# Kernel optimization log

Hardware: AMD Instinct MI355X
Metric: run time of the kernel (lower is better)

Reference implementation:

```python
import jax, jax.numpy as jnp
import numpy as np

V, DM, DEPTH, N = 50257, 512, 8, 16  # vocab, dim, depth, ssm_dim
B, L = 2, 1024
GATE = 0.5  # fixed_gate=True blend


def layer_norm(x, g, b):
    mu = x.mean(-1, keepdims=True)
    xm = x - mu
    var = (xm * xm).mean(-1, keepdims=True)
    return xm * jax.lax.rsqrt(var + 1e-5) * g + b


def ssm(u, W_dt, b_dt, W_B, W_C, A_log, D_p):
    # selective SSM: h_t = exp(dt_t*A)*h_{t-1} + dt_t*B_t*u_t ; y_t = C_t.h_t + D*u_t
    dt = jax.nn.softplus(u @ W_dt + b_dt)            # (B,L,DM)
    Bm = u @ W_B                                      # (B,L,N)
    Cm = u @ W_C                                      # (B,L,N)
    A = -jnp.exp(A_log)                               # (DM,N), stable (negative)

    def step(h, inp):
        dt_t, B_t, C_t, u_t = inp                     # (B,DM),(B,N),(B,N),(B,DM)
        h = jnp.exp(dt_t[..., None] * A) * h + (dt_t * u_t)[..., None] * B_t[:, None, :]
        y = jnp.einsum('bdn,bn->bd', h, C_t)
        return h, y

    h0 = jnp.zeros((u.shape[0], DM, N), u.dtype)
    xs = (dt.transpose(1, 0, 2), Bm.transpose(1, 0, 2), Cm.transpose(1, 0, 2), u.transpose(1, 0, 2))
    _, ys = jax.lax.scan(step, h0, xs)
    return ys.transpose(1, 0, 2) + D_p * u


def wkv(x, W_r, W_k, W_v, W_o, t_decay, t_first):
    # RWKV-4 channel-wise WKV recurrence
    r = jax.nn.sigmoid(x @ W_r)
    k = jnp.clip(x @ W_k, -30.0, 30.0)
    v = x @ W_v
    w = jnp.exp(-jnp.exp(t_decay))                    # (DM,) decay in (0,1)

    def step(carry, inp):
        a, b = carry
        k_t, v_t = inp
        ek = jnp.exp(k_t)
        eu = jnp.exp(t_first + k_t)
        out = (a + eu * v_t) / (b + eu + 1e-6)
        return (w * a + ek * v_t, w * b + ek), out

    a0 = jnp.zeros((x.shape[0], DM), x.dtype)
    _, o = jax.lax.scan(step, (a0, jnp.zeros_like(a0)), (k.transpose(1, 0, 2), v.transpose(1, 0, 2)))
    return (r * o.transpose(1, 0, 2)) @ W_o


def setup_inputs() -> dict:
    key = jax.random.key(0)
    ks = jax.random.split(key, 16)
    s = 0.02
    inp = {
        'input_ids': jax.random.randint(ks[0], (B, L), 0, V, dtype=jnp.int32),
        'emb': jax.random.normal(ks[1], (V, DM), jnp.float32) * s,
        'ln1_g': jnp.ones((DEPTH, DM), jnp.float32),
        'ln1_b': jnp.zeros((DEPTH, DM), jnp.float32),
        'W_dt': jax.random.normal(ks[2], (DEPTH, DM, DM), jnp.float32) * s,
        'b_dt': jnp.zeros((DEPTH, DM), jnp.float32),
        'W_B': jax.random.normal(ks[3], (DEPTH, DM, N), jnp.float32) * s,
        'W_C': jax.random.normal(ks[4], (DEPTH, DM, N), jnp.float32) * s,
        'A_log': jnp.broadcast_to(jnp.log(jnp.arange(1, N + 1, dtype=jnp.float32)), (DEPTH, DM, N)).copy(),
        'D_p': jnp.ones((DEPTH, DM), jnp.float32),
        'ln2_g': jnp.ones((DEPTH, DM), jnp.float32),
        'ln2_b': jnp.zeros((DEPTH, DM), jnp.float32),
        'W_r': jax.random.normal(ks[5], (DEPTH, DM, DM), jnp.float32) * s,
        'W_k': jax.random.normal(ks[6], (DEPTH, DM, DM), jnp.float32) * s,
        'W_v': jax.random.normal(ks[7], (DEPTH, DM, DM), jnp.float32) * s,
        'W_o': jax.random.normal(ks[8], (DEPTH, DM, DM), jnp.float32) * s,
        't_decay': jax.random.normal(ks[9], (DEPTH, DM), jnp.float32) * 0.5,
        't_first': jax.random.normal(ks[10], (DEPTH, DM), jnp.float32) * 0.5,
        'lnf_g': jnp.ones((DM,), jnp.float32),
        'lnf_b': jnp.zeros((DM,), jnp.float32),
    }
    return inp


def reference(input_ids, emb, ln1_g, ln1_b, W_dt, b_dt, W_B, W_C, A_log, D_p,
              ln2_g, ln2_b, W_r, W_k, W_v, W_o, t_decay, t_first, lnf_g, lnf_b):
    x = emb[input_ids]                                # (B,L,DM)
    for i in range(DEPTH):
        x = x + GATE * ssm(layer_norm(x, ln1_g[i], ln1_b[i]),
                           W_dt[i], b_dt[i], W_B[i], W_C[i], A_log[i], D_p[i])
        x = x + GATE * wkv(layer_norm(x, ln2_g[i], ln2_b[i]),
                           W_r[i], W_k[i], W_v[i], W_o[i], t_decay[i], t_first[i])
    x = layer_norm(x, lnf_g, lnf_b)
    logits = x @ emb.T                                # tied LM head, (B,L,V)
    return logits
```

## Files before the change

kernel.cpp:

```cpp
#include <hip/hip_runtime.h>

#define DM 512
#define NST 16
#define NDEPTH 8
#define NB 2
#define NL 1024
#define MROWS 2048
#define VOCAB 50257
#define VPAD  50304
#define NCH 32
#define CLEN 32

typedef __attribute__((ext_vector_type(8))) short bf16x8;
typedef __attribute__((ext_vector_type(4))) float f32x4;
typedef __attribute__((ext_vector_type(8))) unsigned short ushort8;

#define AS1(p) ((const __attribute__((address_space(1))) void*)(p))
#define AS3(p) ((__attribute__((address_space(3))) void*)(p))

static __device__ __forceinline__ unsigned short f2bf(float f) {
  unsigned int x = __float_as_uint(f);
  unsigned int r = (x + 0x7FFFu + ((x >> 16) & 1u)) >> 16;
  return (unsigned short)r;
}
static __device__ __forceinline__ float bf2f(unsigned short u) {
  return __uint_as_float((unsigned int)u << 16);
}

__global__ __launch_bounds__(256) void k_gather(const int* __restrict__ ids,
    const float* __restrict__ emb, float* __restrict__ x)
{
  int gid = blockIdx.x * 256 + threadIdx.x;
  int row = gid >> 7, c = (gid & 127) * 4;
  int id = ids[row];
  *(float4*)(x + (size_t)row * DM + c) = *(const float4*)(emb + (size_t)id * DM + c);
}

__global__ void k_transpose(const float* __restrict__ Wdt, const float* __restrict__ Wr,
    const float* __restrict__ Wk, const float* __restrict__ Wv, const float* __restrict__ Wo,
    unsigned short* __restrict__ Tdtbc, unsigned short* __restrict__ Trkv, unsigned short* __restrict__ To)
{
  __shared__ float tile[32][33];
  int z = blockIdx.z, layer = z / 5, f = z % 5;
  const float* src;
  unsigned short* dst;
  size_t lw = (size_t)layer * DM * DM;
  if (f == 0)      { src = Wdt + lw; dst = Tdtbc + (size_t)layer * 640 * DM; }
  else if (f == 1) { src = Wr  + lw; dst = Trkv + (size_t)layer * 3 * DM * DM; }
  else if (f == 2) { src = Wk  + lw; dst = Trkv + (size_t)layer * 3 * DM * DM + DM * DM; }
  else if (f == 3) { src = Wv  + lw; dst = Trkv + (size_t)layer * 3 * DM * DM + 2 * DM * DM; }
  else             { src = Wo  + lw; dst = To   + lw; }
  int tx = threadIdx.x, ty = threadIdx.y;
  int kb = blockIdx.y * 32, nb = blockIdx.x * 32;
  #pragma unroll
  for (int i = 0; i < 4; i++)
    tile[ty + i * 8][tx] = src[(size_t)(kb + ty + i * 8) * DM + nb + tx];
  __syncthreads();
  #pragma unroll
  for (int i = 0; i < 4; i++)
    dst[(size_t)(nb + ty + i * 8) * DM + kb + tx] = f2bf(tile[tx][ty + i * 8]);
}

__global__ __launch_bounds__(256) void k_bcpack(const float* __restrict__ WB,
    const float* __restrict__ WC, unsigned short* __restrict__ Tdtbc)
{
  int gid = blockIdx.x * 256 + threadIdx.x;
  int k = gid & 511, n = (gid >> 9) & 127, layer = gid >> 16;
  float v = 0.f;
  if (n < 16)      v = WB[((size_t)layer * DM + k) * NST + n];
  else if (n < 32) v = WC[((size_t)layer * DM + k) * NST + (n - 16)];
  Tdtbc[(size_t)layer * 640 * DM + (size_t)(512 + n) * DM + k] = f2bf(v);
}

__global__ __launch_bounds__(256) void k_embcvt(const float* __restrict__ emb,
    unsigned short* __restrict__ out)
{
  int gid = blockIdx.x * 256 + threadIdx.x;
  size_t base = (size_t)gid * 8;
  int row = (int)(base >> 9);
  ushort8 o;
  if (row < VOCAB) {
    float4 a = *(const float4*)(emb + base);
    float4 b = *(const float4*)(emb + base + 4);
    o[0]=f2bf(a.x); o[1]=f2bf(a.y); o[2]=f2bf(a.z); o[3]=f2bf(a.w);
    o[4]=f2bf(b.x); o[5]=f2bf(b.y); o[6]=f2bf(b.z); o[7]=f2bf(b.w);
  } else {
    o = (ushort8)0;
  }
  *(ushort8*)(out + base) = o;
}

__global__ __launch_bounds__(256) void k_ln(const float* __restrict__ x,
    const float* __restrict__ g, const float* __restrict__ bb,
    float* __restrict__ of, unsigned short* __restrict__ ob)
{
  const int w = threadIdx.x >> 6, l = threadIdx.x & 63;
  const int row = blockIdx.x * 4 + w;
  const float* xr = x + (size_t)row * DM + l * 8;
  float4 v0 = *(const float4*)(xr);
  float4 v1 = *(const float4*)(xr + 4);
  float s = v0.x + v0.y + v0.z + v0.w + v1.x + v1.y + v1.z + v1.w;
  float q = v0.x*v0.x + v0.y*v0.y + v0.z*v0.z + v0.w*v0.w
          + v1.x*v1.x + v1.y*v1.y + v1.z*v1.z + v1.w*v1.w;
  #pragma unroll
  for (int m = 1; m < 64; m <<= 1) { s += __shfl_xor(s, m); q += __shfl_xor(q, m); }
  const float mu = s * (1.0f / DM);
  const float var = q * (1.0f / DM) - mu * mu;
  const float rs = rsqrtf(var + 1e-5f);
  const float4 g0 = *(const float4*)(g + l * 8);
  const float4 g1 = *(const float4*)(g + l * 8 + 4);
  const float4 b0 = *(const float4*)(bb + l * 8);
  const float4 b1 = *(const float4*)(bb + l * 8 + 4);
  float y[8];
  y[0] = (v0.x - mu) * rs * g0.x + b0.x;
  y[1] = (v0.y - mu) * rs * g0.y + b0.y;
  y[2] = (v0.z - mu) * rs * g0.z + b0.z;
  y[3] = (v0.w - mu) * rs * g0.w + b0.w;
  y[4] = (v1.x - mu) * rs * g1.x + b1.x;
  y[5] = (v1.y - mu) * rs * g1.y + b1.y;
  y[6] = (v1.z - mu) * rs * g1.z + b1.z;
  y[7] = (v1.w - mu) * rs * g1.w + b1.w;
  if (of) {
    float4 o0 = {y[0], y[1], y[2], y[3]}, o1 = {y[4], y[5], y[6], y[7]};
    *(float4*)(of + (size_t)row * DM + l * 8) = o0;
    *(float4*)(of + (size_t)row * DM + l * 8 + 4) = o1;
  }
  if (ob) {
    ushort8 o;
    #pragma unroll
    for (int j = 0; j < 8; j++) o[j] = f2bf(y[j]);
    *(ushort8*)(ob + (size_t)row * DM + l * 8) = o;
  }
}

template<int BM, int BN, int EPI>
__global__ __launch_bounds__(256) void gemm_bt(const unsigned short* __restrict__ A,
    const unsigned short* __restrict__ Bt, float* __restrict__ C, int N, int ldc,
    const float* __restrict__ bias, float* __restrict__ C2)
{
  constexpr int K = DM;
  constexpr int MI = BM / 32, NI = BN / 32;
  __shared__ unsigned short lsA0[BM * 64];
  __shared__ unsigned short lsA1[BM * 64];
  __shared__ unsigned short lsB0[BN * 64];
  __shared__ unsigned short lsB1[BN * 64];
  const int t = threadIdx.x;
  const int w = t >> 6, l = t & 63;
  const int wm = (w >> 1) * (BM / 2), wn = (w & 1) * (BN / 2);
  const size_t bm = (size_t)blockIdx.x * BM, bn = (size_t)blockIdx.y * BN;
  f32x4 acc[MI][NI] = {};
  const int srow = t >> 3, sslot = t & 7;
  const int gs = sslot ^ (srow & 7);
  const unsigned short* Ag = A + (bm + srow) * K + gs * 8;
  const unsigned short* Bg = Bt + (bn + srow) * K + gs * 8;
  const int lr = l & 15, lq = l >> 4;

#define GB_STAGE(dA, dB, kt) do {                                              \
    const int k0_ = (kt) * 64;                                                 \
    _Pragma("unroll")                                                          \
    for (int o = 0; o < BM / 32; ++o)                                          \
      __builtin_amdgcn_global_load_lds(AS1(Ag + (size_t)(o * 32) * K + k0_),   \
          AS3(dA + (o * 32 + srow) * 64 + sslot * 8), 16, 0, 0);               \
    _Pragma("unroll")                                                          \
    for (int o = 0; o < BN / 32; ++o)                                          \
      __builtin_amdgcn_global_load_lds(AS1(Bg + (size_t)(o * 32) * K + k0_),   \
          AS3(dB + (o * 32 + srow) * 64 + sslot * 8), 16, 0, 0);               \
  } while (0)

#define GB_COMPUTE(sA, sB) do {                                                \
    bf16x8 af[MI][2], bfr[NI][2];                                              \
    _Pragma("unroll")                                                          \
    for (int i = 0; i < MI; ++i) {                                             \
      int row = wm + i * 16 + lr;                                              \
      _Pragma("unroll")                                                        \
      for (int h = 0; h < 2; ++h)                                              \
        af[i][h] = *(const bf16x8*)(sA + row * 64 + (((h * 4 + lq) ^ (row & 7)) * 8)); \
    }                                                                          \
    _Pragma("unroll")                                                          \
    for (int i = 0; i < NI; ++i) {                                             \
      int row = wn + i * 16 + lr;                                              \
      _Pragma("unroll")                                                        \
      for (int h = 0; h < 2; ++h)                                              \
        bfr[i][h] = *(const bf16x8*)(sB + row * 64 + (((h * 4 + lq) ^ (row & 7)) * 8)); \
    }                                                                          \
    _Pragma("unroll")                                                          \
    for (int h = 0; h < 2; ++h)                                                \
      _Pragma("unroll")                                                        \
      for (int mi = 0; mi < MI; ++mi)                                          \
        _Pragma("unroll")                                                      \
        for (int ni = 0; ni < NI; ++ni)                                        \
          acc[mi][ni] = __builtin_amdgcn_mfma_f32_16x16x32_bf16(af[mi][h], bfr[ni][h], acc[mi][ni], 0, 0, 0); \
  } while (0)

  GB_STAGE(lsA0, lsB0, 0);
  __syncthreads();
  #pragma unroll
  for (int kk = 0; kk < 4; ++kk) {
    GB_STAGE(lsA1, lsB1, kk * 2 + 1);
    GB_COMPUTE(lsA0, lsB0);
    __syncthreads();
    if (kk * 2 + 2 < 8) GB_STAGE(lsA0, lsB0, kk * 2 + 2);
    GB_COMPUTE(lsA1, lsB1);
    __syncthreads();
  }
#undef GB_STAGE
#undef GB_COMPUTE

  const int lg = l >> 4;
  #pragma unroll
  for (int mi = 0; mi < MI; ++mi) {
    #pragma unroll
    for (int ni = 0; ni < NI; ++ni) {
      int n = (int)bn + wn + ni * 16 + lr;
      size_t m0 = bm + wm + mi * 16 + lg * 4;
      #pragma unroll
      for (int j = 0; j < 4; ++j) {
        float v = acc[mi][ni][j];
        if (EPI == 0) {
          C[(m0 + j) * (size_t)ldc + n] = v;
        } else if (EPI == 2) {
          C2[(m0 + j) * (size_t)ldc + n] += 0.5f * v;
        } else {
          if (n < 512) {
            float b = v + bias[n];
            C[(m0 + j) * (size_t)512 + n] = fmaxf(b, 0.f) + log1pf(__expf(-fabsf(b)));
          } else if (n < 544) {
            C2[(m0 + j) * (size_t)32 + (n - 512)] = v;
          }
        }
      }
    }
  }
}

__global__ __launch_bounds__(512) void gemm_head(const unsigned short* __restrict__ A,
    const unsigned short* __restrict__ Bt, float* __restrict__ C)
{
  __shared__ unsigned short lsA[256 * 64];
  __shared__ unsigned short lsB[128 * 64];
  const int t = threadIdx.x;
  const int w = t >> 6, l = t & 63;
  const int wm = (w >> 1) * 64, wn = (w & 1) * 64;
  const int c = (int)blockIdx.x & 7, j = (int)blockIdx.x >> 3;
  const int ntile = c * 50 + (j >> 3), mtile = j & 7;
  if (ntile >= 393) return;
  const size_t bm = (size_t)mtile * 256, bn = (size_t)ntile * 128;
  f32x4 acc[4][4] = {};
  const int srow = t >> 3, sslot = t & 7;
  const int gs = sslot ^ (srow & 7);
  const unsigned short* Ag = A + (bm + srow) * DM + gs * 8;
  const unsigned short* Bg = Bt + (bn + srow) * DM + gs * 8;
  const int lr = l & 15, lq = l >> 4;
  for (int k0 = 0; k0 < DM; k0 += 64) {
    #pragma unroll
    for (int o = 0; o < 4; ++o)
      __builtin_amdgcn_global_load_lds(AS1(Ag + (size_t)(o * 64) * DM + k0),
          AS3(lsA + (o * 64 + srow) * 64 + sslot * 8), 16, 0, 0);
    #pragma unroll
    for (int o = 0; o < 2; ++o)
      __builtin_amdgcn_global_load_lds(AS1(Bg + (size_t)(o * 64) * DM + k0),
          AS3(lsB + (o * 64 + srow) * 64 + sslot * 8), 16, 0, 0);
    asm volatile("s_waitcnt vmcnt(0)" ::: "memory");
    __syncthreads();
    bf16x8 af[4][2], bfr[4][2];
    #pragma unroll
    for (int i = 0; i < 4; ++i) {
      int row = wm + i * 16 + lr;
      #pragma unroll
      for (int h = 0; h < 2; ++h)
        af[i][h] = *(const bf16x8*)(lsA + row * 64 + (((h * 4 + lq) ^ (row & 7)) * 8));
    }
    #pragma unroll
    for (int i = 0; i < 4; ++i) {
      int row = wn + i * 16 + lr;
      #pragma unroll
      for (int h = 0; h < 2; ++h)
        bfr[i][h] = *(const bf16x8*)(lsB + row * 64 + (((h * 4 + lq) ^ (row & 7)) * 8));
    }
    #pragma unroll
    for (int h = 0; h < 2; ++h)
      #pragma unroll
      for (int mi = 0; mi < 4; ++mi)
        #pragma unroll
        for (int ni = 0; ni < 4; ++ni)
          acc[mi][ni] = __builtin_amdgcn_mfma_f32_16x16x32_bf16(af[mi][h], bfr[ni][h], acc[mi][ni], 0, 0, 0);
    __syncthreads();
  }
  const int lg = l >> 4;
  #pragma unroll
  for (int mi = 0; mi < 4; ++mi) {
    #pragma unroll
    for (int ni = 0; ni < 4; ++ni) {
      int n = (int)bn + wn + ni * 16 + lr;
      if (n >= VOCAB) continue;
      size_t m0 = bm + wm + mi * 16 + lg * 4;
      #pragma unroll
      for (int jj = 0; jj < 4; ++jj)
        C[(m0 + jj) * (size_t)VOCAB + n] = acc[mi][ni][jj];
    }
  }
}

__global__ __launch_bounds__(256) void k_ssm1(const float* __restrict__ dt,
    const unsigned short* __restrict__ u, const float* __restrict__ BC,
    const float* __restrict__ A_log, float* __restrict__ Pb, float* __restrict__ Sb)
{
  const int t = threadIdx.x;
  const int grp = t >> 4, n = t & 15;
  const int cg = blockIdx.x & 63, ck = blockIdx.x >> 6;
  const int ch = cg * 16 + grp;
  const int b = ch >> 9, d = ch & 511;
  const float A = -__expf(A_log[d * NST + n]);
  const int t0 = ck * CLEN;
  const float* dtp = dt + ((size_t)b * NL + t0) * DM + d;
  const unsigned short* up = u + ((size_t)b * NL + t0) * DM + d;
  const float* bcp = BC + ((size_t)b * NL + t0) * 32 + n;
  float P = 1.f, S = 0.f;
  #pragma unroll
  for (int tt = 0; tt < CLEN; ++tt) {
    float dtv = dtp[(size_t)tt * DM];
    float uv  = bf2f(up[(size_t)tt * DM]);
    float Bv  = bcp[(size_t)tt * 32];
    float e = __expf(dtv * A);
    S = fmaf(e, S, dtv * uv * Bv);
    P *= e;
  }
  size_t cn = (size_t)ch * NST + n;
  Pb[cn * NCH + ck] = P;
  Sb[cn * NCH + ck] = S;
}

__global__ __launch_bounds__(256) void k_ssm2(const float* __restrict__ Pb,
    const float* __restrict__ Sb, float* __restrict__ H0)
{
  const int wid = blockIdx.x * 8 + (threadIdx.x >> 5);
  const int lane = threadIdx.x & 31;
  float coef = Pb[(size_t)wid * NCH + lane];
  float sum  = Sb[(size_t)wid * NCH + lane];
  #pragma unroll
  for (int m = 1; m < 32; m <<= 1) {
    float cr = __shfl_up(coef, m, 32);
    float sr = __shfl_up(sum, m, 32);
    if (lane >= m) { sum = fmaf(coef, sr, sum); coef *= cr; }
  }
  float hp = __shfl_up(sum, 1, 32);
  H0[(size_t)wid * NCH + lane] = (lane == 0) ? 0.f : hp;
}

__global__ __launch_bounds__(256) void k_ssm3(const float* __restrict__ dt,
    const unsigned short* __restrict__ u, const float* __restrict__ BC,
    const float* __restrict__ A_log, const float* __restrict__ Dp,
    const float* __restrict__ H0, float* __restrict__ x)
{
  const int t = threadIdx.x;
  const int grp = t >> 4, n = t & 15;
  const int cg = blockIdx.x & 63, ck = blockIdx.x >> 6;
  const int ch = cg * 16 + grp;
  const int b = ch >> 9, d = ch & 511;
  const float A = -__expf(A_log[d * NST + n]);
  const float Dpv = Dp[d];
  const int t0 = ck * CLEN;
  const float* dtp = dt + ((size_t)b * NL + t0) * DM + d;
  const unsigned short* up = u + ((size_t)b * NL + t0) * DM + d;
  const float* bcp = BC + ((size_t)b * NL + t0) * 32 + n;
  float* xp = x + ((size_t)b * NL + t0) * DM + d;
  size_t cn = (size_t)ch * NST + n;
  float h = H0[cn * NCH + ck];
  #pragma unroll
  for (int tt = 0; tt < CLEN; ++tt) {
    float dtv = dtp[(size_t)tt * DM];
    float uv  = bf2f(up[(size_t)tt * DM]);
    float Bv  = bcp[(size_t)tt * 32];
    float Cv  = bcp[(size_t)tt * 32 + 16];
    float e = __expf(dtv * A);
    h = fmaf(e, h, dtv * uv * Bv);
    float p2 = h * Cv;
    p2 += __shfl_xor(p2, 1);
    p2 += __shfl_xor(p2, 2);
    p2 += __shfl_xor(p2, 4);
    p2 += __shfl_xor(p2, 8);
    if (n == 0) xp[(size_t)tt * DM] += 0.5f * (p2 + Dpv * uv);
  }
}

__global__ __launch_bounds__(256) void k_wkv1(const float* __restrict__ rkv,
    const float* __restrict__ tdec, float* __restrict__ SaB, float* __restrict__ SbB)
{
  const int gid = blockIdx.x * 256 + threadIdx.x;
  const int ch = gid & 1023, ck = gid >> 10;
  const int b = ch >> 9, d = ch & 511;
  const float w = __expf(-__expf(tdec[d]));
  const float* base = rkv + ((size_t)b * NL + ck * CLEN) * 1536;
  float Sa = 0.f, Sb = 0.f;
  #pragma unroll
  for (int tt = 0; tt < CLEN; ++tt) {
    const float* row = base + (size_t)tt * 1536;
    float kt = row[512 + d];
    kt = fminf(30.f, fmaxf(-30.f, kt));
    float vt = row[1024 + d];
    float ek = __expf(kt);
    Sa = fmaf(w, Sa, ek * vt);
    Sb = fmaf(w, Sb, ek);
  }
  SaB[(size_t)ch * NCH + ck] = Sa;
  SbB[(size_t)ch * NCH + ck] = Sb;
}

__global__ __launch_bounds__(256) void k_wkv2(const float* __restrict__ SaB,
    const float* __restrict__ SbB, const float* __restrict__ tdec,
    float* __restrict__ HaB, float* __restrict__ HbB)
{
  const int ch = blockIdx.x * 8 + (threadIdx.x >> 5);
  const int lane = threadIdx.x & 31;
  const int d = ch & 511;
  float coef = __expf(-32.f * __expf(tdec[d]));
  float sa = SaB[(size_t)ch * NCH + lane];
  float sb = SbB[(size_t)ch * NCH + lane];
  #pragma unroll
  for (int m = 1; m < 32; m <<= 1) {
    float cr  = __shfl_up(coef, m, 32);
    float sar = __shfl_up(sa, m, 32);
    float sbr = __shfl_up(sb, m, 32);
    if (lane >= m) { sa = fmaf(coef, sar, sa); sb = fmaf(coef, sbr, sb); coef *= cr; }
  }
  float ha = __shfl_up(sa, 1, 32);
  float hb = __shfl_up(sb, 1, 32);
  HaB[(size_t)ch * NCH + lane] = (lane == 0) ? 0.f : ha;
  HbB[(size_t)ch * NCH + lane] = (lane == 0) ? 0.f : hb;
}

__global__ __launch_bounds__(256) void k_wkv3(const float* __restrict__ rkv,
    const float* __restrict__ tdec, const float* __restrict__ tfir,
    const float* __restrict__ HaB, const float* __restrict__ HbB,
    unsigned short* __restrict__ ro)
{
  const int gid = blockIdx.x * 256 + threadIdx.x;
  const int ch = gid & 1023, ck = gid >> 10;
  const int b = ch >> 9, d = ch & 511;
  const float w = __expf(-__expf(tdec[d]));
  const float tf = tfir[d];
  float a = HaB[(size_t)ch * NCH + ck];
  float bden = HbB[(size_t)ch * NCH + ck];
  const int t0 = ck * CLEN;
  const float* base = rkv + ((size_t)b * NL + t0) * 1536;
  unsigned short* rop = ro + ((size_t)b * NL + t0) * DM + d;
  #pragma unroll
  for (int tt = 0; tt < CLEN; ++tt) {
    const float* row = base + (size_t)tt * 1536;
    float rv = row[d];
    float kt = row[512 + d];
    kt = fminf(30.f, fmaxf(-30.f, kt));
    float vt = row[1024 + d];
    float ek = __expf(kt);
    float eu = __expf(tf + kt);
    float out = __fdividef(a + eu * vt, bden + eu + 1e-6f);
    float sig = __fdividef(1.f, 1.f + __expf(-rv));
    rop[(size_t)tt * DM] = f2bf(sig * out);
    a = fmaf(w, a, ek * vt);
    bden = fmaf(w, bden, ek);
  }
}

extern "C" void kernel_launch(void* const* d_in, const int* in_sizes, int n_in,
                              void* d_out, int out_size, void* d_ws, size_t ws_size,
                              hipStream_t stream)
{
  const int*   ids   = (const int*)d_in[0];
  const float* emb   = (const float*)d_in[1];
  const float* ln1_g = (const float*)d_in[2];
  const float* ln1_b = (const float*)d_in[3];
  const float* W_dt  = (const float*)d_in[4];
  const float* b_dt  = (const float*)d_in[5];
  const float* W_B   = (const float*)d_in[6];
  const float* W_C   = (const float*)d_in[7];
  const float* A_log = (const float*)d_in[8];
  const float* D_p   = (const float*)d_in[9];
  const float* ln2_g = (const float*)d_in[10];
  const float* ln2_b = (const float*)d_in[11];
  const float* W_r   = (const float*)d_in[12];
  const float* W_k   = (const float*)d_in[13];
  const float* W_v   = (const float*)d_in[14];
  const float* W_o   = (const float*)d_in[15];
  const float* t_dec = (const float*)d_in[16];
  const float* t_fir = (const float*)d_in[17];
  const float* lnf_g = (const float*)d_in[18];
  const float* lnf_b = (const float*)d_in[19];

  char* p = (char*)d_ws;
  float*          xres  = (float*)(p + 0);
  float*          dtb   = (float*)(p + 8388608);
  float*          rkv   = (float*)(p + 12582912);
  float*          BCb   = (float*)(p + 25165824);
  unsigned short* abuf  = (unsigned short*)(p + 25427968);
  unsigned short* Tdtbc = (unsigned short*)(p + 27525120);
  unsigned short* To    = (unsigned short*)(p + 32768000);
  unsigned short* Trkv  = (unsigned short*)(p + 36962304);
  unsigned short* Tem   = (unsigned short*)(p + 49545216);

  float* Pb  = rkv;
  float* Sb  = rkv + 524288;
  float* H0  = rkv + 1048576;
  float* SaB = dtb;
  float* SbB = dtb + 32768;
  float* HaB = dtb + 65536;
  float* HbB = dtb + 98304;

  k_gather<<<1024, 256, 0, stream>>>(ids, emb, xres);
  k_transpose<<<dim3(16, 16, 40), dim3(32, 8), 0, stream>>>(W_dt, W_r, W_k, W_v, W_o, Tdtbc, Trkv, To);
  k_bcpack<<<2048, 256, 0, stream>>>(W_B, W_C, Tdtbc);
  k_embcvt<<<12576, 256, 0, stream>>>(emb, Tem);

  for (int i = 0; i < NDEPTH; ++i) {
    k_ln<<<512, 256, 0, stream>>>(xres, ln1_g + i * DM, ln1_b + i * DM, nullptr, abuf);
    gemm_bt<64, 128, 3><<<dim3(32, 5), 256, 0, stream>>>(abuf,
        Tdtbc + (size_t)i * 640 * DM, dtb, 640, 512, b_dt + i * DM, BCb);
    k_ssm1<<<2048, 256, 0, stream>>>(dtb, abuf, BCb, A_log + (size_t)i * DM * NST, Pb, Sb);
    k_ssm2<<<2048, 256, 0, stream>>>(Pb, Sb, H0);
    k_ssm3<<<2048, 256, 0, stream>>>(dtb, abuf, BCb, A_log + (size_t)i * DM * NST,
        D_p + i * DM, H0, xres);
    k_ln<<<512, 256, 0, stream>>>(xres, ln2_g + i * DM, ln2_b + i * DM, nullptr, abuf);
    gemm_bt<64, 128, 0><<<dim3(32, 12), 256, 0, stream>>>(abuf,
        Trkv + (size_t)i * 3 * DM * DM, rkv, 1536, 1536, nullptr, nullptr);
    k_wkv1<<<128, 256, 0, stream>>>(rkv, t_dec + i * DM, SaB, SbB);
    k_wkv2<<<128, 256, 0, stream>>>(SaB, SbB, t_dec + i * DM, HaB, HbB);
    k_wkv3<<<128, 256, 0, stream>>>(rkv, t_dec + i * DM, t_fir + i * DM, HaB, HbB, abuf);
    gemm_bt<64, 128, 2><<<dim3(32, 4), 256, 0, stream>>>(abuf,
        To + (size_t)i * DM * DM, nullptr, 512, 512, nullptr, xres);
  }

  k_ln<<<512, 256, 0, stream>>>(xres, lnf_g, lnf_b, nullptr, abuf);
  gemm_head<<<3200, 512, 0, stream>>>(abuf, Tem, (float*)d_out);
}
```

Before: 1.108 ms.

## Triple-buffer LDS in LM-head GEMM to overlap global loads with MFMA

```diff
diff --git a/kernel.cpp b/kernel.cpp
--- a/kernel.cpp
+++ b/kernel.cpp
@@ -236,8 +236,8 @@
 __global__ __launch_bounds__(512) void gemm_head(const unsigned short* __restrict__ A,
     const unsigned short* __restrict__ Bt, float* __restrict__ C)
 {
-  __shared__ unsigned short lsA[256 * 64];
-  __shared__ unsigned short lsB[128 * 64];
+  __shared__ unsigned short lsA[3][256 * 64];
+  __shared__ unsigned short lsB[3][128 * 64];
   const int t = threadIdx.x;
   const int w = t >> 6, l = t & 63;
   const int wm = (w >> 1) * 64, wn = (w & 1) * 64;
@@ -251,31 +251,42 @@
   const unsigned short* Ag = A + (bm + srow) * DM + gs * 8;
   const unsigned short* Bg = Bt + (bn + srow) * DM + gs * 8;
   const int lr = l & 15, lq = l >> 4;
-  for (int k0 = 0; k0 < DM; k0 += 64) {
-    #pragma unroll
-    for (int o = 0; o < 4; ++o)
-      __builtin_amdgcn_global_load_lds(AS1(Ag + (size_t)(o * 64) * DM + k0),
-          AS3(lsA + (o * 64 + srow) * 64 + sslot * 8), 16, 0, 0);
-    #pragma unroll
-    for (int o = 0; o < 2; ++o)
-      __builtin_amdgcn_global_load_lds(AS1(Bg + (size_t)(o * 64) * DM + k0),
-          AS3(lsB + (o * 64 + srow) * 64 + sslot * 8), 16, 0, 0);
-    asm volatile("s_waitcnt vmcnt(0)" ::: "memory");
-    __syncthreads();
+
+#define H_STAGE(bi, kt) do {                                                   \
+    const int k0_ = (kt) * 64;                                                 \
+    _Pragma("unroll")                                                          \
+    for (int o = 0; o < 4; ++o)                                                \
+      __builtin_amdgcn_global_load_lds(AS1(Ag + (size_t)(o * 64) * DM + k0_),  \
+          AS3(&lsA[bi][(o * 64 + srow) * 64 + sslot * 8]), 16, 0, 0);          \
+    _Pragma("unroll")                                                          \
+    for (int o = 0; o < 2; ++o)                                                \
+      __builtin_amdgcn_global_load_lds(AS1(Bg + (size_t)(o * 64) * DM + k0_),  \
+          AS3(&lsB[bi][(o * 64 + srow) * 64 + sslot * 8]), 16, 0, 0);          \
+  } while (0)
+
+  H_STAGE(0, 0);
+  H_STAGE(1, 1);
+  asm volatile("s_waitcnt vmcnt(6)" ::: "memory");
+  __builtin_amdgcn_s_barrier();
+  for (int kt = 0; kt < 8; ++kt) {
+    const int bi = kt % 3;
+    if (kt + 2 < 8) H_STAGE((kt + 2) % 3, kt + 2);
+    const unsigned short* sA = &lsA[bi][0];
+    const unsigned short* sB = &lsB[bi][0];
     bf16x8 af[4][2], bfr[4][2];
     #pragma unroll
     for (int i = 0; i < 4; ++i) {
       int row = wm + i * 16 + lr;
       #pragma unroll
       for (int h = 0; h < 2; ++h)
-        af[i][h] = *(const bf16x8*)(lsA + row * 64 + (((h * 4 + lq) ^ (row & 7)) * 8));
+        af[i][h] = *(const bf16x8*)(sA + row * 64 + (((h * 4 + lq) ^ (row & 7)) * 8));
     }
     #pragma unroll
     for (int i = 0; i < 4; ++i) {
       int row = wn + i * 16 + lr;
       #pragma unroll
       for (int h = 0; h < 2; ++h)
-        bfr[i][h] = *(const bf16x8*)(lsB + row * 64 + (((h * 4 + lq) ^ (row & 7)) * 8));
+        bfr[i][h] = *(const bf16x8*)(sB + row * 64 + (((h * 4 + lq) ^ (row & 7)) * 8));
     }
     #pragma unroll
     for (int h = 0; h < 2; ++h)
@@ -284,8 +295,12 @@
         #pragma unroll
         for (int ni = 0; ni < 4; ++ni)
           acc[mi][ni] = __builtin_amdgcn_mfma_f32_16x16x32_bf16(af[mi][h], bfr[ni][h], acc[mi][ni], 0, 0, 0);
-    __syncthreads();
-  }
+    if (kt + 2 < 8)      asm volatile("s_waitcnt vmcnt(6)" ::: "memory");
+    else if (kt == 6)    asm volatile("s_waitcnt vmcnt(0)" ::: "memory");
+    __builtin_amdgcn_s_barrier();
+  }
+#undef H_STAGE
+
   const int lg = l >> 4;
   #pragma unroll
   for (int mi = 0; mi < 4; ++mi) {
```

Result: slower. 1.132 ms (+2.2%).
